# Optimization experiments

Hardware: AMD Instinct MI355X
Metric: run time of the kernel (lower is better)

Reference implementation:

```python
import jax, jax.numpy as jnp
import numpy as np
import math

JULIA_ITERS = 64
ESCAPE_RADIUS = 2.0


def _julia_escape_times(seq_len, c_real, c_imag):
    # Positions mapped to the real segment [-2, 2]; iterate z <- z^2 + c,
    # record (first iteration index where |z| > R) / ITERS, else 1.0.
    x = jnp.linspace(-2.0, 2.0, seq_len)
    zr0 = x
    zi0 = jnp.zeros_like(x)
    escaped0 = jnp.zeros(seq_len, dtype=bool)
    et0 = jnp.ones(seq_len, dtype=x.dtype)
    r2 = ESCAPE_RADIUS * ESCAPE_RADIUS

    def step(carry, it):
        zr, zi, escaped, et = carry
        nzr = zr * zr - zi * zi + c_real
        nzi = 2.0 * zr * zi + c_imag
        # torch breaks out of the loop once escaped -> freeze z afterwards
        zr = jnp.where(escaped, zr, nzr)
        zi = jnp.where(escaped, zi, nzi)
        mag2 = zr * zr + zi * zi
        newly = jnp.logical_and(~escaped, mag2 > r2)
        et = jnp.where(newly, it.astype(et.dtype) / JULIA_ITERS, et)
        escaped = jnp.logical_or(escaped, newly)
        return (zr, zi, escaped, et), None

    (_, _, _, et), _ = jax.lax.scan(step, (zr0, zi0, escaped0, et0), jnp.arange(JULIA_ITERS))
    return et


def setup_inputs() -> dict:
    key = jax.random.key(0)
    kq, kk, kv = jax.random.split(key, 3)
    B, S, D = 4, 8192, 64
    return {
        "query": jax.random.normal(kq, (B, S, D), dtype=jnp.float32),
        "key": jax.random.normal(kk, (B, S, D), dtype=jnp.float32),
        "value": jax.random.normal(kv, (B, S, D), dtype=jnp.float32),
        "julia_c_real": jnp.float32(-0.7),
        "julia_c_imag": jnp.float32(0.27),
        "escape_scale": jnp.float32(1.0),
    }


def reference(query, key, value, julia_c_real, julia_c_imag, escape_scale):
    B, S, D = key.shape
    et = _julia_escape_times(S, julia_c_real, julia_c_imag)            # [S]
    julia_weights = jnp.exp(et * escape_scale)                          # [S]
    bias = jnp.log(julia_weights + 1e-8)                                # [S]
    scores = jnp.einsum("bqd,bkd->bqk", query, key) / math.sqrt(D)     # [B,S,S]
    scores = scores + bias[None, None, :]
    attn = jax.nn.softmax(scores, axis=-1)
    out = jnp.einsum("bqk,bkd->bqd", attn, value)                       # [B,S,D]
    return out  # squeeze(1) is a no-op for S > 1
```

## Files before the change

### kernel.cpp

```cpp
#include <hip/hip_runtime.h>
#include <math.h>

#define S_LEN 8192
#define DHEAD 64
#define NBATCH 4
#define BK 32
#define KIT 64

typedef unsigned short u16;
typedef unsigned int u32;
typedef __attribute__((ext_vector_type(8))) _Float16 half8;
typedef __attribute__((ext_vector_type(2))) __fp16 fp16x2;
typedef __attribute__((ext_vector_type(4))) float f32x4;

union HU8 { int4 i4; half8 h8; u32 w[4]; };
union H2U { fp16x2 h2; u32 w; };
union HU  { _Float16 h; u16 u; };

#if __has_builtin(__builtin_amdgcn_exp2f)
#define EXP2(x) __builtin_amdgcn_exp2f(x)
#else
#define EXP2(x) exp2f(x)
#endif

__device__ __forceinline__ u16 f2h(float f) {
    HU x; x.h = (_Float16)f; return x.u;
}
__device__ __forceinline__ u32 packh2(float a, float b) {
    H2U x; x.h2 = __builtin_amdgcn_cvt_pkrtz(a, b); return x.w;
}

__global__ void prep_kernel(const float* __restrict__ K, const float* __restrict__ V,
                            const float* crp, const float* cip, const float* scp,
                            u16* __restrict__ blob, float* __restrict__ bias2) {
    int bid = blockIdx.x, tid = threadIdx.x;
    if (bid < 1024) {
        int b = bid >> 8, t = bid & 255;
        __shared__ float Kt[32 * 64];
        __shared__ float Vt[32 * 65];
        int row = tid >> 3, c8 = (tid & 7) * 8;
        const float* ks = K + ((size_t)(b * S_LEN + t * 32 + row)) * 64 + c8;
        const float* vs = V + ((size_t)(b * S_LEN + t * 32 + row)) * 64 + c8;
        float4 ka = *(const float4*)ks, kb4 = *(const float4*)(ks + 4);
        float4 va = *(const float4*)vs, vb4 = *(const float4*)(vs + 4);
        *(float4*)&Kt[row * 64 + c8] = ka;
        *(float4*)&Kt[row * 64 + c8 + 4] = kb4;
        float* vr = &Vt[row * 65 + c8];
        vr[0] = va.x; vr[1] = va.y; vr[2] = va.z; vr[3] = va.w;
        vr[4] = vb4.x; vr[5] = vb4.y; vr[6] = vb4.z; vr[7] = vb4.w;
        __syncthreads();

        int j = tid >> 6, lane = tid & 63, low = lane & 15, h = lane >> 4;
        u16* tb = blob + ((size_t)(b * 256 + t)) * 4096;
        {
            int kt = j >> 1, ds = j & 1;
            int krow = 8 * (low >> 2) + 4 * kt + (low & 3);
            const float* src = &Kt[krow * 64 + ds * 32 + h * 8];
            u32 wds[4];
#pragma unroll
            for (int i = 0; i < 4; ++i)
                wds[i] = (u32)f2h(src[2 * i]) | ((u32)f2h(src[2 * i + 1]) << 16);
            *(int4*)(tb + j * 512 + lane * 8) = make_int4(wds[0], wds[1], wds[2], wds[3]);
        }
        {
            int col = j * 16 + low;
            u32 wds[4];
#pragma unroll
            for (int i = 0; i < 4; ++i) {
                float a = Vt[(h * 8 + 2 * i) * 65 + col];
                float c = Vt[(h * 8 + 2 * i + 1) * 65 + col];
                wds[i] = (u32)f2h(a) | ((u32)f2h(c) << 16);
            }
            *(int4*)(tb + 2048 + j * 512 + lane * 8) = make_int4(wds[0], wds[1], wds[2], wds[3]);
        }
    } else {
#pragma clang fp contract(off)
        int i = (bid - 1024) * 256 + tid;
        double cr = (double)crp[0], ci = (double)cip[0], sc = (double)scp[0];
        double step = 4.0 / (double)(S_LEN - 1);
        double x = (i == S_LEN - 1) ? 2.0 : (-2.0 + step * (double)i);
        double zr = x, zi = 0.0, et = 1.0;
        bool esc = false;
        for (int it = 0; it < 64; ++it) {
            double nzr = zr * zr - zi * zi + cr;
            double nzi = 2.0 * zr * zi + ci;
            if (!esc) { zr = nzr; zi = nzi; }
            double m2 = zr * zr + zi * zi;
            if (!esc && m2 > 4.0) { et = (double)it / 64.0; esc = true; }
        }
        double bias = log(exp(et * sc) + 1e-8);
        bias2[i] = (float)(bias * 1.4426950408889634 - 20.0);
    }
}

__global__ __launch_bounds__(256, 2)
void flash_kernel(const float* __restrict__ Q, const u16* __restrict__ blob,
                  const float* __restrict__ bias2, float* __restrict__ Out) {
    __shared__ __align__(16) char smem[17664];

    const int tid = threadIdx.x;
    const int l = tid & 63, low = l & 15, h = l >> 4;
    const int kq = __builtin_amdgcn_readfirstlane(tid >> 6);

    const int bid = blockIdx.x;
    const int batch = bid & 3;
    const int qtile = bid >> 2;
    const int q0 = qtile * 64;

    const float qscale = 0.18033688011112042f;
    half8 qfrag[4][2];
#pragma unroll
    for (int qf = 0; qf < 4; ++qf) {
        const float* qrow = Q + ((size_t)(batch * S_LEN + q0 + qf * 16 + low)) * DHEAD + h * 8;
#pragma unroll
        for (int ds = 0; ds < 2; ++ds) {
            f32x4 a = *(const f32x4*)(qrow + ds * 32);
            f32x4 b = *(const f32x4*)(qrow + ds * 32 + 4);
            HU8 u;
            u.w[0] = packh2(a[0] * qscale, a[1] * qscale);
            u.w[1] = packh2(a[2] * qscale, a[3] * qscale);
            u.w[2] = packh2(b[0] * qscale, b[1] * qscale);
            u.w[3] = packh2(b[2] * qscale, b[3] * qscale);
            qfrag[qf][ds] = u.h8;
        }
    }

    const u16* kvb = blob + ((size_t)(batch * 256 + kq * 64)) * 4096;
    const int loff = l * 8;
    const float* bbase = bias2 + kq * 2048;

    f32x4 o[4][4];
#pragma unroll
    for (int qf = 0; qf < 4; ++qf)
#pragma unroll
        for (int dt = 0; dt < 4; ++dt) o[qf][dt] = (f32x4){0, 0, 0, 0};
    float lsum[4] = {0.f, 0.f, 0.f, 0.f};

    HU8 kf[2][4];
    f32x4 bvv[2][2];
    HU8 vf[2][4];
    HU8 pf[4];

    auto QK = [&](const HU8 (&kfc)[4], const f32x4 (&bvc)[2], f32x4 (&st)[2][4]) {
#pragma unroll
        for (int kt = 0; kt < 2; ++kt) {
            const f32x4 binit = bvc[kt];
#pragma unroll
            for (int qf = 0; qf < 4; ++qf) {
                f32x4 a = __builtin_amdgcn_mfma_f32_16x16x32_f16(kfc[kt * 2].h8, qfrag[qf][0], binit, 0, 0, 0);
                a = __builtin_amdgcn_mfma_f32_16x16x32_f16(kfc[kt * 2 + 1].h8, qfrag[qf][1], a, 0, 0, 0);
                st[kt][qf] = a;
            }
        }
    };
    auto SM = [&](const f32x4 (&st)[2][4]) {
#pragma unroll
        for (int kt = 0; kt < 2; ++kt)
#pragma unroll
            for (int qf = 0; qf < 4; ++qf) {
                float p0 = EXP2(st[kt][qf][0]), p1 = EXP2(st[kt][qf][1]);
                float p2 = EXP2(st[kt][qf][2]), p3 = EXP2(st[kt][qf][3]);
                lsum[qf] += (p0 + p1) + (p2 + p3);
                pf[qf].w[kt * 2]     = packh2(p0, p1);
                pf[qf].w[kt * 2 + 1] = packh2(p2, p3);
            }
    };
    auto PV = [&](const HU8 (&vfc)[4]) {
#pragma unroll
        for (int dt = 0; dt < 4; ++dt)
#pragma unroll
            for (int qf = 0; qf < 4; ++qf)
                o[qf][dt] = __builtin_amdgcn_mfma_f32_16x16x32_f16(vfc[dt].h8, pf[qf].h8, o[qf][dt], 0, 0, 0);
    };

#pragma unroll
    for (int j = 0; j < 4; ++j) kf[0][j].i4 = *(const int4*)(kvb + j * 512 + loff);
    bvv[0][0] = *(const f32x4*)(bbase + h * 8);
    bvv[0][1] = *(const f32x4*)(bbase + h * 8 + 4);
#pragma unroll
    for (int j = 0; j < 4; ++j) vf[0][j].i4 = *(const int4*)(kvb + 2048 + j * 512 + loff);
#pragma unroll
    for (int j = 0; j < 4; ++j) kf[1][j].i4 = *(const int4*)(kvb + 4096 + j * 512 + loff);
    bvv[1][0] = *(const f32x4*)(bbase + 32 + h * 8);
    bvv[1][1] = *(const f32x4*)(bbase + 32 + h * 8 + 4);
    {
        f32x4 st0[2][4];
        QK(kf[0], bvv[0], st0);
        SM(st0);
    }

#define BODY(KI, C)                                                              \
    {                                                                            \
        const u16* tb_ = kvb + (size_t)(KI) * 4096;                              \
        _Pragma("unroll")                                                        \
        for (int j = 0; j < 4; ++j)                                              \
            vf[C][j].i4 = *(const int4*)(tb_ + 2048 + j * 512 + loff);           \
        _Pragma("unroll")                                                        \
        for (int j = 0; j < 4; ++j)                                              \
            kf[(C) ^ 1][j].i4 = *(const int4*)(tb_ + 4096 + j * 512 + loff);     \
        const float* bpn_ = bbase + ((KI) + 1) * 32 + h * 8;                     \
        bvv[(C) ^ 1][0] = *(const f32x4*)bpn_;                                   \
        bvv[(C) ^ 1][1] = *(const f32x4*)(bpn_ + 4);                             \
        f32x4 st_[2][4];                                                         \
        QK(kf[C], bvv[C], st_);                                                  \
        PV(vf[(C) ^ 1]);                                                         \
        SM(st_);                                                                 \
    }

#pragma unroll 1
    for (int kp = 1; kp < KIT - 1; kp += 2) {
        BODY(kp, 1)
        BODY(kp + 1, 0)
    }
    BODY(KIT - 1, 1)
    PV(vf[1]);
#undef BODY

#pragma unroll
    for (int qf = 0; qf < 4; ++qf) {
        lsum[qf] += __shfl_xor(lsum[qf], 16, 64);
        lsum[qf] += __shfl_xor(lsum[qf], 32, 64);
    }

    float* MO = (float*)smem;
    float* ML = (float*)(smem + 17408);
#pragma unroll 1
    for (int src = 1; src < 4; ++src) {
        __syncthreads();
        if (kq == src) {
#pragma unroll
            for (int qf = 0; qf < 4; ++qf) {
                const int row = qf * 16 + low;
#pragma unroll
                for (int dt = 0; dt < 4; ++dt)
                    *(f32x4*)&MO[row * 68 + dt * 16 + h * 4] = o[qf][dt];
                if (h == 0) ML[row] = lsum[qf];
            }
        }
        __syncthreads();
        if (kq == 0) {
#pragma unroll
            for (int qf = 0; qf < 4; ++qf) {
                const int row = qf * 16 + low;
#pragma unroll
                for (int dt = 0; dt < 4; ++dt) {
                    f32x4 a = *(const f32x4*)&MO[row * 68 + dt * 16 + h * 4];
#pragma unroll
                    for (int jj = 0; jj < 4; ++jj) o[qf][dt][jj] += a[jj];
                }
                lsum[qf] += ML[row];
            }
        }
    }

    if (kq == 0) {
#pragma unroll
        for (int qf = 0; qf < 4; ++qf) {
            const float inv = 1.f / lsum[qf];
            float* orow = Out + ((size_t)(batch * S_LEN + q0 + qf * 16 + low)) * DHEAD;
#pragma unroll
            for (int dt = 0; dt < 4; ++dt) {
                f32x4 r;
#pragma unroll
                for (int jj = 0; jj < 4; ++jj) r[jj] = o[qf][dt][jj] * inv;
                *(f32x4*)(orow + dt * 16 + h * 4) = r;
            }
        }
    }
}

extern "C" void kernel_launch(void* const* d_in, const int* in_sizes, int n_in,
                              void* d_out, int out_size, void* d_ws, size_t ws_size,
                              hipStream_t stream) {
    const float* Q  = (const float*)d_in[0];
    const float* K  = (const float*)d_in[1];
    const float* V  = (const float*)d_in[2];
    const float* cr = (const float*)d_in[3];
    const float* ci = (const float*)d_in[4];
    const float* sc = (const float*)d_in[5];
    float* out = (float*)d_out;

    char* ws = (char*)d_ws;
    float* bias2 = (float*)ws;
    u16*   blob  = (u16*)(ws + 32768);

    prep_kernel<<<dim3(1056), dim3(256), 0, stream>>>(K, V, cr, ci, sc, blob, bias2);
    flash_kernel<<<dim3(512), dim3(256), 0, stream>>>(Q, blob, bias2, out);
}
```

Baseline: 150.8 us.

## Split key range across eight waves per block with tree reduction of partials

Each block now runs 512 threads (eight waves), and each wave handles half as many key tiles, so the per-wave serial loop is shorter. The cross-wave merge of output and row sums becomes a three-level tree reduction through larger shared memory slots instead of a sequential three-step merge. The cost is more shared memory and heavier register pressure from the new launch bounds, which could cause spills or lower occupancy.

```diff
diff --git a/kernel.cpp b/kernel.cpp
--- a/kernel.cpp
+++ b/kernel.cpp
@@ -5,7 +5,7 @@
 #define DHEAD 64
 #define NBATCH 4
 #define BK 32
-#define KIT 64
+#define KIT 32
 
 typedef unsigned short u16;
 typedef unsigned int u32;
@@ -93,10 +93,10 @@
     }
 }
 
-__global__ __launch_bounds__(256, 2)
+__global__ __launch_bounds__(512, 4)
 void flash_kernel(const float* __restrict__ Q, const u16* __restrict__ blob,
                   const float* __restrict__ bias2, float* __restrict__ Out) {
-    __shared__ __align__(16) char smem[17664];
+    __shared__ __align__(16) char smem[70656];
 
     const int tid = threadIdx.x;
     const int l = tid & 63, low = l & 15, h = l >> 4;
@@ -125,9 +125,9 @@
         }
     }
 
-    const u16* kvb = blob + ((size_t)(batch * 256 + kq * 64)) * 4096;
+    const u16* kvb = blob + ((size_t)(batch * 256 + kq * KIT)) * 4096;
     const int loff = l * 8;
-    const float* bbase = bias2 + kq * 2048;
+    const float* bbase = bias2 + kq * (KIT * 32);
 
     f32x4 o[4][4];
 #pragma unroll
@@ -222,36 +222,47 @@
         lsum[qf] += __shfl_xor(lsum[qf], 32, 64);
     }
 
-    float* MO = (float*)smem;
-    float* ML = (float*)(smem + 17408);
-#pragma unroll 1
-    for (int src = 1; src < 4; ++src) {
-        __syncthreads();
-        if (kq == src) {
-#pragma unroll
-            for (int qf = 0; qf < 4; ++qf) {
-                const int row = qf * 16 + low;
-#pragma unroll
-                for (int dt = 0; dt < 4; ++dt)
-                    *(f32x4*)&MO[row * 68 + dt * 16 + h * 4] = o[qf][dt];
-                if (h == 0) ML[row] = lsum[qf];
-            }
-        }
-        __syncthreads();
-        if (kq == 0) {
-#pragma unroll
-            for (int qf = 0; qf < 4; ++qf) {
-                const int row = qf * 16 + low;
-#pragma unroll
-                for (int dt = 0; dt < 4; ++dt) {
-                    f32x4 a = *(const f32x4*)&MO[row * 68 + dt * 16 + h * 4];
-#pragma unroll
-                    for (int jj = 0; jj < 4; ++jj) o[qf][dt][jj] += a[jj];
-                }
-                lsum[qf] += ML[row];
-            }
-        }
-    }
+    const int FSLOT = 4416;
+    auto wpart = [&](int slot) {
+        float* MO = (float*)smem + slot * FSLOT;
+        float* ML = MO + 4352;
+#pragma unroll
+        for (int qf = 0; qf < 4; ++qf) {
+            const int row = qf * 16 + low;
+#pragma unroll
+            for (int dt = 0; dt < 4; ++dt)
+                *(f32x4*)&MO[row * 68 + dt * 16 + h * 4] = o[qf][dt];
+            if (h == 0) ML[row] = lsum[qf];
+        }
+    };
+    auto apart = [&](int slot) {
+        float* MO = (float*)smem + slot * FSLOT;
+        float* ML = MO + 4352;
+#pragma unroll
+        for (int qf = 0; qf < 4; ++qf) {
+            const int row = qf * 16 + low;
+#pragma unroll
+            for (int dt = 0; dt < 4; ++dt) {
+                f32x4 a = *(const f32x4*)&MO[row * 68 + dt * 16 + h * 4];
+#pragma unroll
+                for (int jj = 0; jj < 4; ++jj) o[qf][dt][jj] += a[jj];
+            }
+            lsum[qf] += ML[row];
+        }
+    };
+
+    __syncthreads();
+    if (kq & 1) wpart(kq >> 1);
+    __syncthreads();
+    if (!(kq & 1)) apart(kq >> 1);
+    __syncthreads();
+    if ((kq & 3) == 2) wpart(kq >> 2);
+    __syncthreads();
+    if ((kq & 3) == 0) apart(kq >> 2);
+    __syncthreads();
+    if (kq == 4) wpart(0);
+    __syncthreads();
+    if (kq == 0) apart(0);
 
     if (kq == 0) {
 #pragma unroll
@@ -285,5 +296,5 @@
     u16*   blob  = (u16*)(ws + 32768);
 
     prep_kernel<<<dim3(1056), dim3(256), 0, stream>>>(K, V, cr, ci, sc, blob, bias2);
-    flash_kernel<<<dim3(512), dim3(256), 0, stream>>>(Q, blob, bias2, out);
-}
+    flash_kernel<<<dim3(512), dim3(512), 0, stream>>>(Q, blob, bias2, out);
+}
```

New measurement: 543.1 us. 260% more time.

## Split key range across two blocks per query tile and merge partial outputs

Applied to the files above, without the earlier changes.

Each query tile's key dimension is split in half across two blocks, doubling the grid from 512 to 1024 blocks. Each block writes unnormalized partial outputs and row sums to workspace, and a new merge kernel combines them and normalizes. The aim is to fill the GPU's compute units better, with occupancy hinted at 4 waves per block slot. The cost is an extra kernel launch plus the extra global memory traffic for the partial outputs. The merge assumes both halves share a fixed max offset, which the bias precompute appears to guarantee.

```diff
diff --git a/kernel.cpp b/kernel.cpp
--- a/kernel.cpp
+++ b/kernel.cpp
@@ -5,7 +5,7 @@
 #define DHEAD 64
 #define NBATCH 4
 #define BK 32
-#define KIT 64
+#define KIT 32
 
 typedef unsigned short u16;
 typedef unsigned int u32;
@@ -93,9 +93,10 @@
     }
 }
 
-__global__ __launch_bounds__(256, 2)
+__global__ __launch_bounds__(256, 4)
 void flash_kernel(const float* __restrict__ Q, const u16* __restrict__ blob,
-                  const float* __restrict__ bias2, float* __restrict__ Out) {
+                  const float* __restrict__ bias2, float* __restrict__ Out,
+                  float* __restrict__ O1, float* __restrict__ LS) {
     __shared__ __align__(16) char smem[17664];
 
     const int tid = threadIdx.x;
@@ -104,7 +105,8 @@
 
     const int bid = blockIdx.x;
     const int batch = bid & 3;
-    const int qtile = bid >> 2;
+    const int khalf = (bid >> 2) & 1;
+    const int qtile = bid >> 3;
     const int q0 = qtile * 64;
 
     const float qscale = 0.18033688011112042f;
@@ -125,9 +127,9 @@
         }
     }
 
-    const u16* kvb = blob + ((size_t)(batch * 256 + kq * 64)) * 4096;
+    const u16* kvb = blob + ((size_t)(batch * 256 + khalf * 128 + kq * KIT)) * 4096;
     const int loff = l * 8;
-    const float* bbase = bias2 + kq * 2048;
+    const float* bbase = bias2 + khalf * 4096 + kq * (KIT * 32);
 
     f32x4 o[4][4];
 #pragma unroll
@@ -254,19 +256,33 @@
     }
 
     if (kq == 0) {
+        float* OP = khalf ? O1 : Out;
 #pragma unroll
         for (int qf = 0; qf < 4; ++qf) {
-            const float inv = 1.f / lsum[qf];
-            float* orow = Out + ((size_t)(batch * S_LEN + q0 + qf * 16 + low)) * DHEAD;
-#pragma unroll
-            for (int dt = 0; dt < 4; ++dt) {
-                f32x4 r;
-#pragma unroll
-                for (int jj = 0; jj < 4; ++jj) r[jj] = o[qf][dt][jj] * inv;
-                *(f32x4*)(orow + dt * 16 + h * 4) = r;
-            }
-        }
-    }
+            const int row = q0 + qf * 16 + low;
+            float* orow = OP + ((size_t)(batch * S_LEN + row)) * DHEAD;
+#pragma unroll
+            for (int dt = 0; dt < 4; ++dt)
+                *(f32x4*)(orow + dt * 16 + h * 4) = o[qf][dt];
+            if (h == 0)
+                LS[khalf * 32768 + batch * S_LEN + row] = lsum[qf];
+        }
+    }
+}
+
+__global__ __launch_bounds__(256)
+void merge_kernel(float* __restrict__ Out, const float* __restrict__ O1,
+                  const float* __restrict__ LS) {
+    const int idx = blockIdx.x * 256 + threadIdx.x;
+    const int rowg = idx >> 4;
+    const float l0 = LS[rowg], l1 = LS[32768 + rowg];
+    const float inv = 1.f / (l0 + l1);
+    f32x4 a = *(const f32x4*)(Out + (size_t)idx * 4);
+    f32x4 c = *(const f32x4*)(O1 + (size_t)idx * 4);
+    f32x4 r;
+#pragma unroll
+    for (int jj = 0; jj < 4; ++jj) r[jj] = (a[jj] + c[jj]) * inv;
+    *(f32x4*)(Out + (size_t)idx * 4) = r;
 }
 
 extern "C" void kernel_launch(void* const* d_in, const int* in_sizes, int n_in,
@@ -283,7 +299,10 @@
     char* ws = (char*)d_ws;
     float* bias2 = (float*)ws;
     u16*   blob  = (u16*)(ws + 32768);
+    float* O1    = (float*)(ws + 8429568);
+    float* LS    = (float*)(ws + 16818176);
 
     prep_kernel<<<dim3(1056), dim3(256), 0, stream>>>(K, V, cr, ci, sc, blob, bias2);
-    flash_kernel<<<dim3(512), dim3(256), 0, stream>>>(Q, blob, bias2, out);
-}
+    flash_kernel<<<dim3(1024), dim3(256), 0, stream>>>(Q, blob, bias2, out, O1, LS);
+    merge_kernel<<<dim3(2048), dim3(256), 0, stream>>>(out, O1, LS);
+}
```

Result: slower. 531.3 us (+252.4%).
